# Kernel tuning notes

Measured on AMD Instinct MI355X. Metric: run time of the kernel, lower is better.

Reference implementation:

```python
import jax, jax.numpy as jnp
import numpy as np

B, A, N = 8, 512, 64           # structures, atoms, neighbors
D, F, G = 128, 128, 25         # atom basis, filters, gaussians
L = 3                          # interaction blocks
GA = 512                       # angular feature dim = 2*n_zetas*2*n_angular*n_zetas
MAXZ = 100
CUTOFF, START = 5.0, 1.2
LN2 = 0.6931471805599453


def ssp(x):
    # shifted softplus: ln(1+exp(x)) - ln(2)
    return jax.nn.softplus(x) - LN2


def setup_inputs() -> dict:
    key = jax.random.key(0)
    ks = jax.random.split(key, 16)
    atomic_numbers = jax.random.randint(ks[0], (B, A), 0, MAXZ, dtype=jnp.int32)
    positions = jax.random.normal(ks[1], (B, A, 3), dtype=jnp.float32) * 3.0
    neighbors = jax.random.randint(ks[2], (B, A, N), 0, A, dtype=jnp.int32)
    neighbor_mask = jax.random.randint(ks[3], (B, A, N), 0, 2, dtype=jnp.int32)
    G_i = jax.random.normal(ks[4], (B, A, GA), dtype=jnp.float32)
    s = 0.05
    embedding = jax.random.normal(ks[5], (MAXZ, D), dtype=jnp.float32) * 0.1
    embedding = embedding.at[0].set(0.0)  # padding_idx=0
    inp = {
        'atomic_numbers': atomic_numbers,
        'positions': positions,
        'neighbors': neighbors,
        'neighbor_mask': neighbor_mask,
        'G_i': G_i,
        'embedding': embedding,
        'filt_w1': jax.random.normal(ks[6], (L, G, F), dtype=jnp.float32) * s,
        'filt_b1': jnp.zeros((L, F), jnp.float32),
        'filt_w2': jax.random.normal(ks[7], (L, F, F), dtype=jnp.float32) * s,
        'filt_b2': jnp.zeros((L, F), jnp.float32),
        'in2f_w': jax.random.normal(ks[8], (L, D, F), dtype=jnp.float32) * s,
        'f2out_w': jax.random.normal(ks[9], (L, F, D), dtype=jnp.float32) * s,
        'f2out_b': jnp.zeros((L, D), jnp.float32),
        'dense_w': jax.random.normal(ks[10], (L, D, D), dtype=jnp.float32) * s,
        'dense_b': jnp.zeros((L, D), jnp.float32),
        'ang_w': jax.random.normal(ks[11], (L, GA, D), dtype=jnp.float32) * s,
    }
    return inp


def reference(atomic_numbers, positions, neighbors, neighbor_mask, G_i,
              embedding, filt_w1, filt_b1, filt_w2, filt_b2,
              in2f_w, f2out_w, f2out_b, dense_w, dense_b, ang_w):
    gather = jax.vmap(lambda feat, idx: feat[idx])  # per-structure neighbor gather

    x = embedding[atomic_numbers]                    # [B,A,D]

    # AtomDistances: gather neighbor positions and take pairwise norms
    pos_j = gather(positions, neighbors)             # [B,A,N,3]
    dvec = pos_j - positions[:, :, None, :]
    r_ij = jnp.sqrt(jnp.sum(dvec * dvec, axis=-1) + 1e-12)  # [B,A,N]

    # GaussianSmearing(start, cutoff, n_gaussians)
    offsets = jnp.linspace(START, CUTOFF, G).astype(x.dtype)
    width = offsets[1] - offsets[0]
    f_ij = jnp.exp((-0.5 / (width * width)) * (r_ij[..., None] - offsets) ** 2)  # [B,A,N,G]

    C = (r_ij <= CUTOFF).astype(x.dtype)             # HardCutoff [B,A,N]
    mask = neighbor_mask.astype(x.dtype)             # [B,A,N]

    for l in range(in2f_w.shape[0]):
        # filter-generating network on expanded distances, modulated by cutoff
        W = ssp(f_ij @ filt_w1[l] + filt_b1[l]) @ filt_w2[l] + filt_b2[l]  # [B,A,N,F]
        W = W * C[..., None]
        # CFConv: project, gather neighbors, filter-weight, masked neighbor sum
        y = x @ in2f_w[l]                            # [B,A,F]
        y_j = gather(y, neighbors)                   # [B,A,N,F]
        agg = jnp.sum(y_j * W * mask[..., None], axis=2)  # [B,A,F]
        v_rad = agg @ f2out_w[l] + f2out_b[l]        # f2out (activation=None)
        v_rad = v_rad @ dense_w[l] + dense_b[l]      # self.dense
        v_ang = G_i @ ang_w[l]                       # dense_angular (no bias)
        x = x + ssp(v_rad + v_ang)                   # residual interaction update
    return x
```

## Files before the change

### kernel.cpp

```cpp
#include <hip/hip_runtime.h>
#include <math.h>

#define NB 8
#define NA 512
#define NN 64
#define ND 128
#define NF 128
#define NG 25
#define NGA 512
#define TABN 1024

typedef __attribute__((ext_vector_type(8))) short bf16x8;
typedef __attribute__((ext_vector_type(4))) float f32x4;

__device__ __forceinline__ float sspf(float v) {
  return fmaxf(v, 0.0f) + __logf(1.0f + __expf(-fabsf(v))) - 0.6931471805599453f;
}

__device__ __forceinline__ short f2bf(float x) {
  union { float f; unsigned u; } v; v.f = x;
  unsigned r = v.u + 0x7fffu + ((v.u >> 16) & 1u);
  return (short)(r >> 16);
}

#if defined(__has_builtin)
#if __has_builtin(__builtin_amdgcn_cvt_pk_bf16_f32)
#define HAS_PKBF 1
#endif
#endif

__device__ __forceinline__ unsigned pk2bf(float a, float b) {
#ifdef HAS_PKBF
  typedef __attribute__((ext_vector_type(2))) __bf16 v2bf;
  union { v2bf v; unsigned u; } c;
  c.v = __builtin_amdgcn_cvt_pk_bf16_f32(a, b);
  return c.u;
#else
  union { float f; unsigned u; } x, y; x.f = a; y.f = b;
  const unsigned ra = (x.u + 0x7fffu + ((x.u >> 16) & 1u)) >> 16;
  const unsigned rb = (y.u + 0x7fffu + ((y.u >> 16) & 1u)) & 0xffff0000u;
  return ra | rb;
#endif
}

__device__ __forceinline__ float bf2f(unsigned short us) {
  union { unsigned u; float f; } v; v.u = ((unsigned)us) << 16; return v.f;
}

__device__ __forceinline__ bf16x8 pack8(float4 a, float4 b) {
  bf16x8 r;
  unsigned* p = (unsigned*)&r;
  p[0] = pk2bf(a.x, a.y); p[1] = pk2bf(a.z, a.w);
  p[2] = pk2bf(b.x, b.y); p[3] = pk2bf(b.z, b.w);
  return r;
}

__device__ __forceinline__ bf16x8 fragT(const float* __restrict__ M, int ldn,
                                        int n, int k0q) {
  float e[8];
#pragma unroll
  for (int i = 0; i < 8; ++i) e[i] = M[(size_t)(k0q + i) * ldn + n];
  bf16x8 r; unsigned* p = (unsigned*)&r;
  p[0] = pk2bf(e[0], e[1]); p[1] = pk2bf(e[2], e[3]);
  p[2] = pk2bf(e[4], e[5]); p[3] = pk2bf(e[6], e[7]);
  return r;
}

__device__ __forceinline__ bf16x8 fragT25(const float* __restrict__ M,
                                          int n, int k0q) {
  float e[8];
#pragma unroll
  for (int i = 0; i < 8; ++i)
    e[i] = (k0q + i < NG) ? M[(size_t)(k0q + i) * NF + n] : 0.0f;
  bf16x8 r; unsigned* p = (unsigned*)&r;
  p[0] = pk2bf(e[0], e[1]); p[1] = pk2bf(e[2], e[3]);
  p[2] = pk2bf(e[4], e[5]); p[3] = pk2bf(e[6], e[7]);
  return r;
}

#define B_TT 48
#define B_AT (B_TT + 192)
#define B_PF (B_AT + 24)
#define B_TAB (B_PF + 192)
#define P1_TOT (B_TAB + 1024)

#define P2_VA 768
#define P2_TOT (P2_VA + 256)

__global__ __launch_bounds__(256) void k_prep1(
    const float* __restrict__ fw1, const float* __restrict__ fb1,
    const float* __restrict__ fw2, const float* __restrict__ fb2,
    const float* __restrict__ in2f, const float* __restrict__ aw,
    const float* __restrict__ f2o, const float* __restrict__ f2ob,
    const float* __restrict__ dw, const float* __restrict__ db,
    const float* __restrict__ pos, const int* __restrict__ nbr,
    const int* __restrict__ nmask,
    short* __restrict__ in2fT, short* __restrict__ awT,
    short* __restrict__ W12T, float* __restrict__ b12,
    float* __restrict__ Ttab, int4* __restrict__ ent,
    int* __restrict__ nvArr) {
  __shared__ alignas(16) short sTile[32][33];
  __shared__ alignas(16) short sH[16 * 136];
  __shared__ alignas(16) int4 sCmp[4][NN];
  const int bx = blockIdx.x;
  const int t = threadIdx.x;
  const int lane = t & 63, wave = t >> 6;
  const int lanelo = lane & 15, quad = lane >> 4;
  const int wbase = wave << 5;

  if (bx < B_AT) {
    const float* src; short* dst; int tk0, tn0, stride;
    if (bx < B_TT) {
      const int l = bx >> 4, tile = bx & 15;
      src = in2f + (size_t)l * 16384;
      dst = in2fT + (size_t)l * 16384;
      tk0 = (tile >> 2) << 5; tn0 = (tile & 3) << 5; stride = 128;
    } else {
      const int ab = bx - B_TT;
      const int l = ab >> 6, tile = ab & 63;
      src = aw + (size_t)l * 65536;
      dst = awT + (size_t)l * 65536;
      tk0 = (tile >> 2) << 5; tn0 = (tile & 3) << 5; stride = 512;
    }
    const int tr = t >> 3, tc4 = (t & 7) << 2;
    const float4 v = *(const float4*)(src + (size_t)(tk0 + tr) * 128 + tn0 + tc4);
    sTile[tr][tc4] = f2bf(v.x); sTile[tr][tc4 + 1] = f2bf(v.y);
    sTile[tr][tc4 + 2] = f2bf(v.z); sTile[tr][tc4 + 3] = f2bf(v.w);
    __syncthreads();
    short o[4];
#pragma unroll
    for (int j = 0; j < 4; ++j) o[j] = sTile[tc4 + j][tr];
    uint2 pk;
    pk.x = ((unsigned)(unsigned short)o[0]) | (((unsigned)(unsigned short)o[1]) << 16);
    pk.y = ((unsigned)(unsigned short)o[2]) | (((unsigned)(unsigned short)o[3]) << 16);
    *(uint2*)(dst + (size_t)(tn0 + tr) * stride + tk0 + tc4) = pk;
    return;
  }
  if (bx < B_PF) {
    const int fb = bx - B_AT;
    const int l = fb >> 3, xi = fb & 7;
    const int i = (xi << 4) + lanelo;
    const float* f2o_l = f2o + (size_t)l * 16384;
    const float* dw_l = dw + (size_t)l * 16384;
    short* W12T_l = W12T + (size_t)l * 16384;
    f32x4 c[2] = {{0.f, 0.f, 0.f, 0.f}, {0.f, 0.f, 0.f, 0.f}};
#pragma unroll
    for (int kt = 0; kt < 4; ++kt) {
      const int k0 = kt * 32 + quad * 8;
      const bf16x8 b = pack8(*(const float4*)(f2o_l + (size_t)i * 128 + k0),
                             *(const float4*)(f2o_l + (size_t)i * 128 + k0 + 4));
#pragma unroll
      for (int ct = 0; ct < 2; ++ct) {
        const bf16x8 a = fragT(dw_l, 128, wbase + ct * 16 + lanelo, k0);
        c[ct] = __builtin_amdgcn_mfma_f32_16x16x32_bf16(a, b, c[ct], 0, 0, 0);
      }
    }
#pragma unroll
    for (int ct = 0; ct < 2; ++ct)
#pragma unroll
      for (int reg = 0; reg < 4; ++reg) {
        const int j = wbase + ct * 16 + quad * 4 + reg;
        W12T_l[(size_t)j * 128 + i] = f2bf(c[ct][reg]);
      }
    if (xi == 0 && t < 128) {
      float acc = db[(size_t)l * 128 + t];
      for (int k = 0; k < 128; ++k)
        acc += f2ob[(size_t)l * 128 + k] * dw_l[(size_t)k * 128 + t];
      b12[(size_t)l * 128 + t] = acc;
    }
    return;
  }
  if (bx < B_TAB) {
    const int tb = bx - B_PF;
    const int l = tb >> 6;
    const int chunk = tb & 63;
    const float* fw1_l = fw1 + (size_t)l * NG * NF;
    const float* fw2_l = fw2 + (size_t)l * 16384;
    const float* b1 = fb1 + (size_t)l * NF;
    const float* b2 = fb2 + (size_t)l * NF;

    float4 b1v[2];
    float b2r[2];
#pragma unroll
    for (int ct = 0; ct < 2; ++ct) {
      b1v[ct] = *(const float4*)(b1 + wbase + ct * 16 + quad * 4);
      b2r[ct] = b2[wbase + ct * 16 + lanelo];
    }

    const float stepg = 3.8f / 24.0f;
    const float coef = -0.5f / (stepg * stepg);
    const float rv = (float)(chunk * 16 + lanelo) * (5.0f / 1023.0f);
    bf16x8 gb;
    {
      float e[8];
#pragma unroll
      for (int i = 0; i < 8; ++i) {
        const int g = quad * 8 + i;
        const float d = rv - (1.2f + stepg * (float)g);
        e[i] = (g < NG) ? __expf(coef * d * d) : 0.0f;
      }
      unsigned* gp = (unsigned*)&gb;
      gp[0] = pk2bf(e[0], e[1]); gp[1] = pk2bf(e[2], e[3]);
      gp[2] = pk2bf(e[4], e[5]); gp[3] = pk2bf(e[6], e[7]);
    }
#pragma unroll
    for (int ct = 0; ct < 2; ++ct) {
      const bf16x8 a = fragT25(fw1_l, wbase + ct * 16 + lanelo, quad * 8);
      f32x4 c = {0.f, 0.f, 0.f, 0.f};
      c = __builtin_amdgcn_mfma_f32_16x16x32_bf16(a, gb, c, 0, 0, 0);
      const int f0 = wbase + ct * 16 + quad * 4;
      uint2 pk;
      pk.x = pk2bf(sspf(c[0] + b1v[ct].x), sspf(c[1] + b1v[ct].y));
      pk.y = pk2bf(sspf(c[2] + b1v[ct].z), sspf(c[3] + b1v[ct].w));
      *(uint2*)(sH + lanelo * 136 + f0) = pk;
    }
    __syncthreads();
    f32x4 acc[2];
    acc[0] = (f32x4){b2r[0], b2r[0], b2r[0], b2r[0]};
    acc[1] = (f32x4){b2r[1], b2r[1], b2r[1], b2r[1]};
#pragma unroll
    for (int kt = 0; kt < 4; ++kt) {
      const bf16x8 ah = *(const bf16x8*)(sH + lanelo * 136 + kt * 32 + quad * 8);
#pragma unroll
      for (int ct = 0; ct < 2; ++ct) {
        const bf16x8 a = fragT(fw2_l, 128, wbase + ct * 16 + lanelo, kt * 32 + quad * 8);
        acc[ct] = __builtin_amdgcn_mfma_f32_16x16x32_bf16(ah, a, acc[ct], 0, 0, 0);
      }
    }
#pragma unroll
    for (int ct = 0; ct < 2; ++ct)
#pragma unroll
      for (int reg = 0; reg < 4; ++reg) {
        const int rrow = chunk * 16 + quad * 4 + reg;
        const int f = wbase + ct * 16 + lanelo;
        Ttab[((size_t)l * TABN + rrow) * NF + f] = acc[ct][reg];
      }
    return;
  }
  {
    const int ga = (bx - B_TAB) * 4 + wave;
    const int b0 = ga & ~(NA - 1);
    const int nj = nbr[(size_t)ga * NN + lane];
    const int mk = nmask[(size_t)ga * NN + lane];
    const float px = pos[(size_t)ga * 3];
    const float py = pos[(size_t)ga * 3 + 1];
    const float pz = pos[(size_t)ga * 3 + 2];
    const float* pj = pos + (size_t)(b0 + nj) * 3;
    const float dx = pj[0] - px, dy = pj[1] - py, dz = pj[2] - pz;
    const float r = sqrtf(dx * dx + dy * dy + dz * dz + 1e-12f);
    const bool valid = (r <= 5.0f) && (mk != 0);
    const unsigned long long m = __ballot(valid);
    const int posc = __popcll(m & ((1ull << lane) - 1ull));
    const float tt = r * ((float)(TABN - 1) / 5.0f);
    int k0 = (int)tt; if (k0 > TABN - 2) k0 = TABN - 2;
    const float fr = tt - (float)k0;
    sCmp[wave][lane] = make_int4(0, b0 * NF, 0, 0);
    if (valid)
      sCmp[wave][posc] = make_int4(k0 * NF, (b0 + nj) * NF,
                                   __float_as_int(1.0f - fr), __float_as_int(fr));
    ent[(size_t)ga * NN + lane] = sCmp[wave][lane];
    if (lane == 0) nvArr[ga] = (int)__popcll(m);
  }
}

__global__ __launch_bounds__(256) void k_prep2(
    const float* __restrict__ emb, const int* __restrict__ zn,
    const float* __restrict__ Gi, const short* __restrict__ awT,
    const short* __restrict__ in2fT,
    short* __restrict__ vangB, float* __restrict__ x, short* __restrict__ yB) {
  const int bx = blockIdx.x;
  const int t = threadIdx.x;
  const int lane = t & 63, wave = t >> 6;
  const int lanelo = lane & 15, quad = lane >> 4;
  const int wbase = wave << 5;

  if (bx < P2_VA) {
    const int l = bx >> 8;
    const int row = ((bx & 255) << 4) + lanelo;
    const short* awT_l = awT + (size_t)l * 65536;
    const float* grow = Gi + (size_t)row * NGA;
    f32x4 c[2] = {{0.f, 0.f, 0.f, 0.f}, {0.f, 0.f, 0.f, 0.f}};
#pragma unroll
    for (int kt = 0; kt < 16; ++kt) {
      const int k0 = kt * 32 + quad * 8;
      const bf16x8 b = pack8(*(const float4*)(grow + k0),
                             *(const float4*)(grow + k0 + 4));
#pragma unroll
      for (int ct = 0; ct < 2; ++ct) {
        const bf16x8 a = *(const bf16x8*)(awT_l + (size_t)(wbase + ct * 16 + lanelo) * 512 + k0);
        c[ct] = __builtin_amdgcn_mfma_f32_16x16x32_bf16(a, b, c[ct], 0, 0, 0);
      }
    }
    short* vrow = vangB + ((size_t)l * NB * NA + row) * 128;
#pragma unroll
    for (int ct = 0; ct < 2; ++ct) {
      uint2 pk; pk.x = pk2bf(c[ct][0], c[ct][1]); pk.y = pk2bf(c[ct][2], c[ct][3]);
      *(uint2*)(vrow + wbase + ct * 16 + quad * 4) = pk;
    }
    return;
  }
  {
    const int row = ((bx - P2_VA) << 4) + lanelo;
    const float* erow = emb + (size_t)zn[row] * ND;
    f32x4 c[2] = {{0.f, 0.f, 0.f, 0.f}, {0.f, 0.f, 0.f, 0.f}};
#pragma unroll
    for (int kt = 0; kt < 4; ++kt) {
      const int k0 = kt * 32 + quad * 8;
      const float4 e0 = *(const float4*)(erow + k0);
      const float4 e1 = *(const float4*)(erow + k0 + 4);
      if (wave == 0) {
        *(float4*)(x + (size_t)row * ND + k0) = e0;
        *(float4*)(x + (size_t)row * ND + k0 + 4) = e1;
      }
      const bf16x8 b = pack8(e0, e1);
#pragma unroll
      for (int ct = 0; ct < 2; ++ct) {
        const bf16x8 a = *(const bf16x8*)(in2fT + (size_t)(wbase + ct * 16 + lanelo) * 128 + k0);
        c[ct] = __builtin_amdgcn_mfma_f32_16x16x32_bf16(a, b, c[ct], 0, 0, 0);
      }
    }
#pragma unroll
    for (int ct = 0; ct < 2; ++ct) {
      const int c0 = wbase + ct * 16 + quad * 4;
      uint2 pk; pk.x = pk2bf(c[ct][0], c[ct][1]); pk.y = pk2bf(c[ct][2], c[ct][3]);
      *(uint2*)(yB + (size_t)row * 128 + c0) = pk;
    }
  }
}

__global__ __launch_bounds__(512) void k_layer(
    const short* __restrict__ yIn, const float* __restrict__ Tt,
    float* __restrict__ x, const short* __restrict__ vangL,
    const short* __restrict__ W12Tl, const float* __restrict__ b12l,
    const short* __restrict__ in2fTn, short* __restrict__ yOut,
    const int4* __restrict__ ent, const int* __restrict__ nvArr) {
  __shared__ alignas(16) int4 sEnt[8][NN];
  __shared__ alignas(16) float sAgg[16][136];
  __shared__ alignas(16) short sT[16 * 136];

  const int t = threadIdx.x;
  const int lane = t & 63;
  const int wave = t >> 6;
  const int lanelo = lane & 15;
  const int quad = lane >> 4;
  const int ga0 = blockIdx.x << 3;

  sEnt[wave][lane] = ent[(size_t)(ga0 + wave) * NN + lane];
  const int nv = nvArr[ga0 + wave];

  const unsigned short* yu = (const unsigned short*)yIn;
  float acc0 = 0.f, acc1 = 0.f;
  const int ntc = (nv + 3) & ~3;
  for (int c = 0; c < ntc; c += 4) {
#pragma unroll
    for (int u = 0; u < 4; ++u) {
      const int4 e = sEnt[wave][c + u];
      const float w0 = __int_as_float(e.z), w1 = __int_as_float(e.w);
      const float t0a = Tt[e.x + lane];
      const float t0b = Tt[e.x + lane + 64];
      const float t1a = Tt[e.x + NF + lane];
      const float t1b = Tt[e.x + NF + lane + 64];
      const float wva = fmaf(w0, t0a, w1 * t1a);
      const float wvb = fmaf(w0, t0b, w1 * t1b);
      acc0 = fmaf(wva, bf2f(yu[e.y + lane]), acc0);
      acc1 = fmaf(wvb, bf2f(yu[e.y + lane + 64]), acc1);
    }
  }
  sAgg[wave][lane] = acc0;
  sAgg[wave][lane + 64] = acc1;
  __syncthreads();

  f32x4 c2 = {0.f, 0.f, 0.f, 0.f};
#pragma unroll
  for (int kt = 0; kt < 4; ++kt) {
    const float* ar = &sAgg[lanelo][kt * 32 + quad * 8];
    const bf16x8 b = pack8(*(const float4*)ar, *(const float4*)(ar + 4));
    const bf16x8 a = *(const bf16x8*)(W12Tl + ((wave << 4) + lanelo) * 128 + kt * 32 + quad * 8);
    c2 = __builtin_amdgcn_mfma_f32_16x16x32_bf16(a, b, c2, 0, 0, 0);
  }

  const int c0 = (wave << 4) + quad * 4;
  const int row = ga0 + lanelo;
  if (lanelo < 8) {
    const float4 dv = *(const float4*)(b12l + c0);
    const unsigned short* vp = (const unsigned short*)(vangL + (size_t)row * 128 + c0);
    float* xp = x + (size_t)row * 128 + c0;
    const float4 xv = *(const float4*)xp;
    float4 xo;
    xo.x = xv.x + sspf(c2[0] + bf2f(vp[0]) + dv.x);
    xo.y = xv.y + sspf(c2[1] + bf2f(vp[1]) + dv.y);
    xo.z = xv.z + sspf(c2[2] + bf2f(vp[2]) + dv.z);
    xo.w = xv.w + sspf(c2[3] + bf2f(vp[3]) + dv.w);
    *(float4*)xp = xo;
    if (in2fTn != nullptr) {
      uint2 pk; pk.x = pk2bf(xo.x, xo.y); pk.y = pk2bf(xo.z, xo.w);
      *(uint2*)(sT + lanelo * 136 + c0) = pk;
    }
  }
  if (in2fTn == nullptr) return;
  __syncthreads();

  f32x4 c3 = {0.f, 0.f, 0.f, 0.f};
#pragma unroll
  for (int kt = 0; kt < 4; ++kt) {
    const bf16x8 b = *(const bf16x8*)(sT + lanelo * 136 + kt * 32 + quad * 8);
    const bf16x8 a = *(const bf16x8*)(in2fTn + ((wave << 4) + lanelo) * 128 + kt * 32 + quad * 8);
    c3 = __builtin_amdgcn_mfma_f32_16x16x32_bf16(a, b, c3, 0, 0, 0);
  }
  if (lanelo < 8) {
    uint2 pk; pk.x = pk2bf(c3[0], c3[1]); pk.y = pk2bf(c3[2], c3[3]);
    *(uint2*)(yOut + (size_t)row * 128 + c0) = pk;
  }
}

extern "C" void kernel_launch(void* const* d_in, const int* in_sizes, int n_in,
                              void* d_out, int out_size, void* d_ws, size_t ws_size,
                              hipStream_t stream) {
  (void)in_sizes; (void)n_in; (void)out_size; (void)ws_size;
  const int* zn = (const int*)d_in[0];
  const float* pos = (const float*)d_in[1];
  const int* nbr = (const int*)d_in[2];
  const int* nmask = (const int*)d_in[3];
  const float* Gi = (const float*)d_in[4];
  const float* emb = (const float*)d_in[5];
  const float* fw1 = (const float*)d_in[6];
  const float* fb1 = (const float*)d_in[7];
  const float* fw2 = (const float*)d_in[8];
  const float* fb2 = (const float*)d_in[9];
  const float* in2f = (const float*)d_in[10];
  const float* f2o = (const float*)d_in[11];
  const float* f2ob = (const float*)d_in[12];
  const float* dwp = (const float*)d_in[13];
  const float* dbp = (const float*)d_in[14];
  const float* awp = (const float*)d_in[15];

  float* x = (float*)d_out;
  float* b12 = (float*)d_ws;
  float* Ttab = b12 + 3 * 128;
  short* vangB = (short*)(Ttab + (size_t)3 * TABN * NF);
  short* yA = vangB + (size_t)3 * NB * NA * ND;
  short* yBb = yA + (size_t)NB * NA * NF;
  short* in2fT = yBb + (size_t)NB * NA * NF;
  short* W12T = in2fT + (size_t)3 * 128 * 128;
  short* awT = W12T + (size_t)3 * 128 * 128;
  int4* ent = (int4*)(awT + (size_t)3 * 128 * 512);
  int* nvArr = (int*)(ent + (size_t)NB * NA * NN);

  k_prep1<<<P1_TOT, 256, 0, stream>>>(
      fw1, fb1, fw2, fb2, in2f, awp, f2o, f2ob, dwp, dbp,
      pos, nbr, nmask,
      in2fT, awT, W12T, b12, Ttab, ent, nvArr);
  k_prep2<<<P2_TOT, 256, 0, stream>>>(
      emb, zn, Gi, awT, in2fT, vangB, x, yA);

  short* yin = yA;
  short* yout = yBb;
  for (int l = 0; l < 3; ++l) {
    k_layer<<<NB * NA / 8, 512, 0, stream>>>(yin,
        Ttab + (size_t)l * TABN * NF,
        x, vangB + (size_t)l * NB * NA * ND,
        W12T + (size_t)l * 16384, b12 + (size_t)l * 128,
        (l < 2) ? (in2fT + (size_t)(l + 1) * 16384) : nullptr, yout,
        ent, nvArr);
    short* tmp = yin; yin = yout; yout = tmp;
  }
}
```

Baseline: 149.7 us.

## Fuse angular projection G_i@ang_w into per-layer kernel, drop vang buffer

Moves the angular dense projection out of the prep kernel and into each layer kernel. Each block stages its 8 rows of G_i as bf16 in shared memory and accumulates them into the same MFMA accumulator as the radial path. This removes the precomputed vang buffer and its global write and read traffic, and shrinks the prep kernel. In exchange each layer reloads G_i and the 128x512 angular weights per block, adds 16 MFMA steps per wave, and raises shared memory use; launch bounds now also request 4 blocks per CU.

```diff
diff --git a/kernel.cpp b/kernel.cpp
--- a/kernel.cpp
+++ b/kernel.cpp
@@ -83,9 +83,6 @@
 #define B_PF (B_AT + 24)
 #define B_TAB (B_PF + 192)
 #define P1_TOT (B_TAB + 1024)
-
-#define P2_VA 768
-#define P2_TOT (P2_VA + 256)
 
 __global__ __launch_bounds__(256) void k_prep1(
     const float* __restrict__ fw1, const float* __restrict__ fb1,
@@ -265,78 +262,52 @@
 
 __global__ __launch_bounds__(256) void k_prep2(
     const float* __restrict__ emb, const int* __restrict__ zn,
-    const float* __restrict__ Gi, const short* __restrict__ awT,
     const short* __restrict__ in2fT,
-    short* __restrict__ vangB, float* __restrict__ x, short* __restrict__ yB) {
+    float* __restrict__ x, short* __restrict__ yB) {
   const int bx = blockIdx.x;
   const int t = threadIdx.x;
   const int lane = t & 63, wave = t >> 6;
   const int lanelo = lane & 15, quad = lane >> 4;
   const int wbase = wave << 5;
 
-  if (bx < P2_VA) {
-    const int l = bx >> 8;
-    const int row = ((bx & 255) << 4) + lanelo;
-    const short* awT_l = awT + (size_t)l * 65536;
-    const float* grow = Gi + (size_t)row * NGA;
-    f32x4 c[2] = {{0.f, 0.f, 0.f, 0.f}, {0.f, 0.f, 0.f, 0.f}};
-#pragma unroll
-    for (int kt = 0; kt < 16; ++kt) {
-      const int k0 = kt * 32 + quad * 8;
-      const bf16x8 b = pack8(*(const float4*)(grow + k0),
-                             *(const float4*)(grow + k0 + 4));
-#pragma unroll
-      for (int ct = 0; ct < 2; ++ct) {
-        const bf16x8 a = *(const bf16x8*)(awT_l + (size_t)(wbase + ct * 16 + lanelo) * 512 + k0);
-        c[ct] = __builtin_amdgcn_mfma_f32_16x16x32_bf16(a, b, c[ct], 0, 0, 0);
-      }
-    }
-    short* vrow = vangB + ((size_t)l * NB * NA + row) * 128;
+  const int row = (bx << 4) + lanelo;
+  const float* erow = emb + (size_t)zn[row] * ND;
+  f32x4 c[2] = {{0.f, 0.f, 0.f, 0.f}, {0.f, 0.f, 0.f, 0.f}};
+#pragma unroll
+  for (int kt = 0; kt < 4; ++kt) {
+    const int k0 = kt * 32 + quad * 8;
+    const float4 e0 = *(const float4*)(erow + k0);
+    const float4 e1 = *(const float4*)(erow + k0 + 4);
+    if (wave == 0) {
+      *(float4*)(x + (size_t)row * ND + k0) = e0;
+      *(float4*)(x + (size_t)row * ND + k0 + 4) = e1;
+    }
+    const bf16x8 b = pack8(e0, e1);
 #pragma unroll
     for (int ct = 0; ct < 2; ++ct) {
-      uint2 pk; pk.x = pk2bf(c[ct][0], c[ct][1]); pk.y = pk2bf(c[ct][2], c[ct][3]);
-      *(uint2*)(vrow + wbase + ct * 16 + quad * 4) = pk;
-    }
-    return;
-  }
-  {
-    const int row = ((bx - P2_VA) << 4) + lanelo;
-    const float* erow = emb + (size_t)zn[row] * ND;
-    f32x4 c[2] = {{0.f, 0.f, 0.f, 0.f}, {0.f, 0.f, 0.f, 0.f}};
-#pragma unroll
-    for (int kt = 0; kt < 4; ++kt) {
-      const int k0 = kt * 32 + quad * 8;
-      const float4 e0 = *(const float4*)(erow + k0);
-      const float4 e1 = *(const float4*)(erow + k0 + 4);
-      if (wave == 0) {
-        *(float4*)(x + (size_t)row * ND + k0) = e0;
-        *(float4*)(x + (size_t)row * ND + k0 + 4) = e1;
-      }
-      const bf16x8 b = pack8(e0, e1);
-#pragma unroll
-      for (int ct = 0; ct < 2; ++ct) {
-        const bf16x8 a = *(const bf16x8*)(in2fT + (size_t)(wbase + ct * 16 + lanelo) * 128 + k0);
-        c[ct] = __builtin_amdgcn_mfma_f32_16x16x32_bf16(a, b, c[ct], 0, 0, 0);
-      }
-    }
-#pragma unroll
-    for (int ct = 0; ct < 2; ++ct) {
-      const int c0 = wbase + ct * 16 + quad * 4;
-      uint2 pk; pk.x = pk2bf(c[ct][0], c[ct][1]); pk.y = pk2bf(c[ct][2], c[ct][3]);
-      *(uint2*)(yB + (size_t)row * 128 + c0) = pk;
-    }
-  }
-}
-
-__global__ __launch_bounds__(512) void k_layer(
+      const bf16x8 a = *(const bf16x8*)(in2fT + (size_t)(wbase + ct * 16 + lanelo) * 128 + k0);
+      c[ct] = __builtin_amdgcn_mfma_f32_16x16x32_bf16(a, b, c[ct], 0, 0, 0);
+    }
+  }
+#pragma unroll
+  for (int ct = 0; ct < 2; ++ct) {
+    const int c0 = wbase + ct * 16 + quad * 4;
+    uint2 pk; pk.x = pk2bf(c[ct][0], c[ct][1]); pk.y = pk2bf(c[ct][2], c[ct][3]);
+    *(uint2*)(yB + (size_t)row * 128 + c0) = pk;
+  }
+}
+
+__global__ __launch_bounds__(512, 4) void k_layer(
     const short* __restrict__ yIn, const float* __restrict__ Tt,
-    float* __restrict__ x, const short* __restrict__ vangL,
+    const float* __restrict__ Gi, const short* __restrict__ awTl,
+    float* __restrict__ x,
     const short* __restrict__ W12Tl, const float* __restrict__ b12l,
     const short* __restrict__ in2fTn, short* __restrict__ yOut,
     const int4* __restrict__ ent, const int* __restrict__ nvArr) {
   __shared__ alignas(16) int4 sEnt[8][NN];
   __shared__ alignas(16) float sAgg[16][136];
   __shared__ alignas(16) short sT[16 * 136];
+  __shared__ alignas(16) short sGi[8][520];
 
   const int t = threadIdx.x;
   const int lane = t & 63;
@@ -344,6 +315,13 @@
   const int lanelo = lane & 15;
   const int quad = lane >> 4;
   const int ga0 = blockIdx.x << 3;
+
+  {
+    const int r = t >> 6, cc = (t & 63) << 3;
+    const float* g = Gi + (size_t)(ga0 + r) * NGA + cc;
+    const bf16x8 v = pack8(*(const float4*)g, *(const float4*)(g + 4));
+    *(bf16x8*)(&sGi[r][cc]) = v;
+  }
 
   sEnt[wave][lane] = ent[(size_t)(ga0 + wave) * NN + lane];
   const int nv = nvArr[ga0 + wave];
@@ -378,19 +356,25 @@
     const bf16x8 a = *(const bf16x8*)(W12Tl + ((wave << 4) + lanelo) * 128 + kt * 32 + quad * 8);
     c2 = __builtin_amdgcn_mfma_f32_16x16x32_bf16(a, b, c2, 0, 0, 0);
   }
+#pragma unroll 4
+  for (int kt = 0; kt < 16; ++kt) {
+    const int k0 = kt * 32 + quad * 8;
+    const bf16x8 a = *(const bf16x8*)(awTl + (size_t)((wave << 4) + lanelo) * 512 + k0);
+    const bf16x8 b = *(const bf16x8*)(&sGi[lanelo & 7][k0]);
+    c2 = __builtin_amdgcn_mfma_f32_16x16x32_bf16(a, b, c2, 0, 0, 0);
+  }
 
   const int c0 = (wave << 4) + quad * 4;
   const int row = ga0 + lanelo;
   if (lanelo < 8) {
     const float4 dv = *(const float4*)(b12l + c0);
-    const unsigned short* vp = (const unsigned short*)(vangL + (size_t)row * 128 + c0);
     float* xp = x + (size_t)row * 128 + c0;
     const float4 xv = *(const float4*)xp;
     float4 xo;
-    xo.x = xv.x + sspf(c2[0] + bf2f(vp[0]) + dv.x);
-    xo.y = xv.y + sspf(c2[1] + bf2f(vp[1]) + dv.y);
-    xo.z = xv.z + sspf(c2[2] + bf2f(vp[2]) + dv.z);
-    xo.w = xv.w + sspf(c2[3] + bf2f(vp[3]) + dv.w);
+    xo.x = xv.x + sspf(c2[0] + dv.x);
+    xo.y = xv.y + sspf(c2[1] + dv.y);
+    xo.z = xv.z + sspf(c2[2] + dv.z);
+    xo.w = xv.w + sspf(c2[3] + dv.w);
     *(float4*)xp = xo;
     if (in2fTn != nullptr) {
       uint2 pk; pk.x = pk2bf(xo.x, xo.y); pk.y = pk2bf(xo.z, xo.w);
@@ -437,8 +421,7 @@
   float* x = (float*)d_out;
   float* b12 = (float*)d_ws;
   float* Ttab = b12 + 3 * 128;
-  short* vangB = (short*)(Ttab + (size_t)3 * TABN * NF);
-  short* yA = vangB + (size_t)3 * NB * NA * ND;
+  short* yA = (short*)(Ttab + (size_t)3 * TABN * NF);
   short* yBb = yA + (size_t)NB * NA * NF;
   short* in2fT = yBb + (size_t)NB * NA * NF;
   short* W12T = in2fT + (size_t)3 * 128 * 128;
@@ -450,16 +433,16 @@
       fw1, fb1, fw2, fb2, in2f, awp, f2o, f2ob, dwp, dbp,
       pos, nbr, nmask,
       in2fT, awT, W12T, b12, Ttab, ent, nvArr);
-  k_prep2<<<P2_TOT, 256, 0, stream>>>(
-      emb, zn, Gi, awT, in2fT, vangB, x, yA);
+  k_prep2<<<NB * NA / 16, 256, 0, stream>>>(
+      emb, zn, in2fT, x, yA);
 
   short* yin = yA;
   short* yout = yBb;
   for (int l = 0; l < 3; ++l) {
     k_layer<<<NB * NA / 8, 512, 0, stream>>>(yin,
         Ttab + (size_t)l * TABN * NF,
-        x, vangB + (size_t)l * NB * NA * ND,
-        W12T + (size_t)l * 16384, b12 + (size_t)l * 128,
+        Gi, awT + (size_t)l * 65536,
+        x, W12T + (size_t)l * 16384, b12 + (size_t)l * 128,
         (l < 2) ? (in2fT + (size_t)(l + 1) * 16384) : nullptr, yout,
         ent, nvArr);
     short* tmp = yin; yin = yout; yout = tmp;
```

Result: no change. 151.7 us (+1.3%).
